# Performance work log

Hardware: AMD Instinct MI355X
Metric: run time of the kernel (lower is better)

## Reference

```python
import jax, jax.numpy as jnp
import numpy as np

NEG_INF = float(np.finfo(np.float32).min)


def setup_inputs() -> dict:
    key = jax.random.key(0)
    k1, k2, k3 = jax.random.split(key, 3)
    n_context, d_model = 4096, 2048
    x = jax.random.normal(k1, (n_context, d_model), dtype=jnp.float32)
    # nn.Linear default init scale ~ 1/sqrt(fan_in); use small weights for numeric sanity
    W_qk = jax.random.normal(k2, (d_model, d_model), dtype=jnp.float32) / np.sqrt(d_model)
    W_ov = jax.random.normal(k3, (d_model, d_model), dtype=jnp.float32) / np.sqrt(d_model)
    return {"x": x, "W_qk": W_qk, "W_ov": W_ov}


def reference(x, W_qk, W_ov):
    # Faithful to: softmax(X @ W_qk.T @ X.T + causal_mask) @ X @ W_ov.T
    # (biases of the torch Linears are never used in forward)
    n = x.shape[0]
    q = x @ W_qk.T                      # [n, d]
    scores = q @ x.T                    # [n, n]  (no 1/sqrt(d) scaling, as in source)
    causal = jnp.tril(jnp.ones((n, n), dtype=bool))
    scores = jnp.where(causal, scores, NEG_INF)  # additive -inf mask equivalent
    attn = jax.nn.softmax(scores, axis=-1)       # [n, n]
    out = (attn @ x) @ W_ov.T                    # [n, d]
    return out
```

## Files before the change

kernel.cpp:

```cpp
#include <hip/hip_runtime.h>
#include <hip/hip_bf16.h>
#include <stdint.h>
#include <stddef.h>
#include <math.h>

typedef _Float16 f16;
typedef __attribute__((ext_vector_type(8))) _Float16 f16x8;
typedef __attribute__((ext_vector_type(4))) float    f32x4;

constexpr int BM = 128, BN = 128, BK = 64;

#define GLOAD_LDS16(gp, lp)                                        \
    __builtin_amdgcn_global_load_lds(                              \
        (const __attribute__((address_space(1))) unsigned int*)(gp),\
        (__attribute__((address_space(3))) unsigned int*)(lp), 16, 0, 0)

#define MFMA_TILE(AV, BV)                                                     \
    do {                                                                      \
        __builtin_amdgcn_s_setprio(1);                                        \
        _Pragma("unroll")                                                     \
        for (int mi_ = 0; mi_ < 4; ++mi_)                                     \
            _Pragma("unroll")                                                 \
            for (int ni_ = 0; ni_ < 4; ++ni_)                                 \
                acc[mi_][ni_] = __builtin_amdgcn_mfma_f32_16x16x32_f16(       \
                    (AV)[mi_], (BV)[ni_], acc[mi_][ni_], 0, 0, 0);            \
        __builtin_amdgcn_s_setprio(0);                                        \
    } while (0)

#define SGB __builtin_amdgcn_sched_group_barrier

template <int EPI>
__global__ __launch_bounds__(512, 2) void gemm8_a2(
    const f16* __restrict__ Ah, const f16* __restrict__ Al,
    const f16* __restrict__ B,
    float* __restrict__ Cf, f16* __restrict__ Co, f16* __restrict__ Clo,
    int M, int N, int K)
{
    const int gx  = gridDim.x;
    const int nwg = gx * gridDim.y;
    const int id  = blockIdx.y * gx + blockIdx.x;
    const int cpx = nwg >> 3;
    const int j   = (id & 7) * cpx + (id >> 3);
    const int bx  = j % gx;
    const int by  = j / gx;

    const int tid   = threadIdx.x;
    const int lane  = tid & 63;
    const int wave  = tid >> 6;
    const int wm    = wave >> 2;
    const int wn    = wave & 3;
    const int lrow  = lane & 15;
    const int lquad = lane >> 4;

    __shared__ f16 lds[2][32768];

    const int row0 = by * 128;
    const int col0 = bx * 256;

    const int srow = tid >> 3;
    const int scol = ((tid & 7) ^ (srow & 7)) * 8;
    const int loff = wave * 512;

    const int g0 = ((lquad)     ^ (lrow & 7)) * 8;
    const int g1 = ((4 + lquad) ^ (lrow & 7)) * 8;

    const int arow = (wm * 64 + lrow) * 64;
    const int brow = (wn * 64 + lrow) * 64 + 16384;

    const f16* gAh = Ah + (size_t)(row0 + srow) * K + scol;
    const f16* gAl = Al + (size_t)(row0 + srow) * K + scol;
    const f16* gB  = B  + (size_t)(col0 + srow) * K + scol;
    const size_t r64 = (size_t)64 * K;

    f32x4 acc[4][4];
    const f32x4 fz = {0.f, 0.f, 0.f, 0.f};
    #pragma unroll
    for (int i = 0; i < 4; ++i)
        #pragma unroll
        for (int jj = 0; jj < 4; ++jj) acc[i][jj] = fz;

    const int nt = K / 64;

    #pragma unroll
    for (int u = 0; u < 4; ++u)
        GLOAD_LDS16(gB + u * r64, &lds[0][16384 + u * 4096 + loff]);
    #pragma unroll
    for (int u = 0; u < 2; ++u)
        GLOAD_LDS16(gAh + u * r64, &lds[0][u * 4096 + loff]);
    #pragma unroll
    for (int u = 0; u < 2; ++u)
        GLOAD_LDS16(gAl + u * r64, &lds[0][8192 + u * 4096 + loff]);
    asm volatile("s_waitcnt vmcnt(0)");
    __builtin_amdgcn_s_barrier();

    for (int t = 0; t < nt; ++t) {
        const f16* bufc = &lds[t & 1][0];
        f16* bufn = &lds[(t + 1) & 1][0];
        const size_t kn = (size_t)((t + 1 < nt) ? t + 1 : t) * 64;

        f16x8 ah0[4], ah1[4], al0[4], al1[4], bv0[4], bv1[4];

        #pragma unroll
        for (int mi = 0; mi < 4; ++mi)
            ah0[mi] = *(const f16x8*)&bufc[arow + mi * 1024 + g0];
        #pragma unroll
        for (int ni = 0; ni < 4; ++ni)
            bv0[ni] = *(const f16x8*)&bufc[brow + ni * 1024 + g0];

        GLOAD_LDS16(gB + kn,           &bufn[16384 + loff]);
        GLOAD_LDS16(gB + r64 + kn,     &bufn[16384 +  4096 + loff]);
        GLOAD_LDS16(gB + 2 * r64 + kn, &bufn[16384 +  8192 + loff]);
        GLOAD_LDS16(gB + 3 * r64 + kn, &bufn[16384 + 12288 + loff]);
        GLOAD_LDS16(gAh + kn,          &bufn[loff]);
        GLOAD_LDS16(gAh + r64 + kn,    &bufn[4096 + loff]);
        GLOAD_LDS16(gAl + kn,          &bufn[ 8192 + loff]);
        GLOAD_LDS16(gAl + r64 + kn,    &bufn[12288 + loff]);

        #pragma unroll
        for (int mi = 0; mi < 4; ++mi)
            ah1[mi] = *(const f16x8*)&bufc[arow + mi * 1024 + g1];
        #pragma unroll
        for (int ni = 0; ni < 4; ++ni)
            bv1[ni] = *(const f16x8*)&bufc[brow + ni * 1024 + g1];

        MFMA_TILE(ah0, bv0);

        #pragma unroll
        for (int mi = 0; mi < 4; ++mi)
            al0[mi] = *(const f16x8*)&bufc[8192 + arow + mi * 1024 + g0];

        MFMA_TILE(ah1, bv1);

        #pragma unroll
        for (int mi = 0; mi < 4; ++mi)
            al1[mi] = *(const f16x8*)&bufc[8192 + arow + mi * 1024 + g1];

        MFMA_TILE(al0, bv0);
        MFMA_TILE(al1, bv1);

        SGB(0x100, 8, 0);
        SGB(0x20,  8, 0);
        SGB(0x100, 8, 0);
        SGB(0x8,  16, 0);
        SGB(0x100, 4, 0);
        SGB(0x8,  16, 0);
        SGB(0x100, 4, 0);
        SGB(0x8,  32, 0);

        asm volatile("s_waitcnt vmcnt(0)");
        __builtin_amdgcn_s_barrier();
    }

    #pragma unroll
    for (int mi = 0; mi < 4; ++mi) {
        #pragma unroll
        for (int ni = 0; ni < 4; ++ni) {
            #pragma unroll
            for (int r = 0; r < 4; ++r) {
                const int row = row0 + wm * 64 + mi * 16 + lquad * 4 + r;
                const int col = col0 + wn * 64 + ni * 16 + lrow;
                const size_t idx = (size_t)row * N + col;
                const float v = acc[mi][ni][r];
                if (EPI == 0) {
                    Cf[idx] = v;
                } else {
                    const f16 h = (f16)v;
                    Co[idx]  = h;
                    Clo[idx] = (f16)(v - (float)h);
                }
            }
        }
    }
}

__global__ __launch_bounds__(512, 2) void gemm8_s_jobs(
    const f16* __restrict__ Ah, const f16* __restrict__ Al,
    const f16* __restrict__ B,
    float* __restrict__ Cf, int N, int K)
{
    const int b = blockIdx.x;
    const int j = (b & 7) * 32 + (b >> 3);
    int r = (int)sqrtf((float)j);
    while (r * r > j) --r;
    while ((r + 1) * (r + 1) <= j) ++r;
    const int u = j - r * r;
    const int by = (u < r) ? 2 * r : 2 * r + 1;
    const int bx = (u < r) ? u : u - r;

    const int tid   = threadIdx.x;
    const int lane  = tid & 63;
    const int wave  = tid >> 6;
    const int wm    = wave >> 2;
    const int wn    = wave & 3;
    const int lrow  = lane & 15;
    const int lquad = lane >> 4;

    __shared__ f16 lds[2][32768];

    const int row0 = by * 128;
    const int col0 = bx * 256;

    const int srow = tid >> 3;
    const int scol = ((tid & 7) ^ (srow & 7)) * 8;
    const int loff = wave * 512;

    const int g0 = ((lquad)     ^ (lrow & 7)) * 8;
    const int g1 = ((4 + lquad) ^ (lrow & 7)) * 8;

    const int arow = (wm * 64 + lrow) * 64;
    const int brow = (wn * 64 + lrow) * 64 + 16384;

    const f16* gAh = Ah + (size_t)(row0 + srow) * K + scol;
    const f16* gAl = Al + (size_t)(row0 + srow) * K + scol;
    const f16* gB  = B  + (size_t)(col0 + srow) * K + scol;
    const size_t r64 = (size_t)64 * K;

    f32x4 acc[4][4];
    const f32x4 fz = {0.f, 0.f, 0.f, 0.f};
    #pragma unroll
    for (int i = 0; i < 4; ++i)
        #pragma unroll
        for (int jj = 0; jj < 4; ++jj) acc[i][jj] = fz;

    const int nt = K / 64;

    #pragma unroll
    for (int u2 = 0; u2 < 4; ++u2)
        GLOAD_LDS16(gB + u2 * r64, &lds[0][16384 + u2 * 4096 + loff]);
    #pragma unroll
    for (int u2 = 0; u2 < 2; ++u2)
        GLOAD_LDS16(gAh + u2 * r64, &lds[0][u2 * 4096 + loff]);
    #pragma unroll
    for (int u2 = 0; u2 < 2; ++u2)
        GLOAD_LDS16(gAl + u2 * r64, &lds[0][8192 + u2 * 4096 + loff]);
    asm volatile("s_waitcnt vmcnt(0)");
    __builtin_amdgcn_s_barrier();

    for (int t = 0; t < nt; ++t) {
        const f16* bufc = &lds[t & 1][0];
        f16* bufn = &lds[(t + 1) & 1][0];
        const size_t kn = (size_t)((t + 1 < nt) ? t + 1 : t) * 64;

        f16x8 ah0[4], ah1[4], al0[4], al1[4], bv0[4], bv1[4];

        #pragma unroll
        for (int mi = 0; mi < 4; ++mi)
            ah0[mi] = *(const f16x8*)&bufc[arow + mi * 1024 + g0];
        #pragma unroll
        for (int ni = 0; ni < 4; ++ni)
            bv0[ni] = *(const f16x8*)&bufc[brow + ni * 1024 + g0];

        GLOAD_LDS16(gB + kn,           &bufn[16384 + loff]);
        GLOAD_LDS16(gB + r64 + kn,     &bufn[16384 +  4096 + loff]);
        GLOAD_LDS16(gB + 2 * r64 + kn, &bufn[16384 +  8192 + loff]);
        GLOAD_LDS16(gB + 3 * r64 + kn, &bufn[16384 + 12288 + loff]);
        GLOAD_LDS16(gAh + kn,          &bufn[loff]);
        GLOAD_LDS16(gAh + r64 + kn,    &bufn[4096 + loff]);
        GLOAD_LDS16(gAl + kn,          &bufn[ 8192 + loff]);
        GLOAD_LDS16(gAl + r64 + kn,    &bufn[12288 + loff]);

        #pragma unroll
        for (int mi = 0; mi < 4; ++mi)
            ah1[mi] = *(const f16x8*)&bufc[arow + mi * 1024 + g1];
        #pragma unroll
        for (int ni = 0; ni < 4; ++ni)
            bv1[ni] = *(const f16x8*)&bufc[brow + ni * 1024 + g1];

        MFMA_TILE(ah0, bv0);

        #pragma unroll
        for (int mi = 0; mi < 4; ++mi)
            al0[mi] = *(const f16x8*)&bufc[8192 + arow + mi * 1024 + g0];

        MFMA_TILE(ah1, bv1);

        #pragma unroll
        for (int mi = 0; mi < 4; ++mi)
            al1[mi] = *(const f16x8*)&bufc[8192 + arow + mi * 1024 + g1];

        MFMA_TILE(al0, bv0);
        MFMA_TILE(al1, bv1);

        SGB(0x100, 8, 0);
        SGB(0x20,  8, 0);
        SGB(0x100, 8, 0);
        SGB(0x8,  16, 0);
        SGB(0x100, 4, 0);
        SGB(0x8,  16, 0);
        SGB(0x100, 4, 0);
        SGB(0x8,  32, 0);

        asm volatile("s_waitcnt vmcnt(0)");
        __builtin_amdgcn_s_barrier();
    }

    #pragma unroll
    for (int mi = 0; mi < 4; ++mi) {
        #pragma unroll
        for (int ni = 0; ni < 4; ++ni) {
            #pragma unroll
            for (int rr = 0; rr < 4; ++rr) {
                const int row = row0 + wm * 64 + mi * 16 + lquad * 4 + rr;
                const int col = col0 + wn * 64 + ni * 16 + lrow;
                Cf[(size_t)row * N + col] = acc[mi][ni][rr];
            }
        }
    }
}

__global__ __launch_bounds__(256) void gemm_half_splitk(
    const f16* __restrict__ Ah, const f16* __restrict__ Al,
    const f16* __restrict__ B, float* __restrict__ Spart, int Kg)
{
    const int kc = blockIdx.x;
    const int h  = blockIdx.y;
    const int row0 = h * 256;
    const int kbeg = kc * 256;

    const int tid   = threadIdx.x;
    const int lane  = tid & 63;
    const int wave  = tid >> 6;
    const int wm    = wave >> 1;
    const int wn    = wave & 1;
    const int lrow  = lane & 15;
    const int lquad = lane >> 4;

    __shared__ f16 sAh[BM * BK];
    __shared__ f16 sAl[BM * BK];
    __shared__ f16 sB [BM * BK];

    const int srow = tid >> 3;
    const int scol = (((tid & 7) ^ ((tid >> 3) & 7))) * 8;
    const int lbase = wave * 512;

    f32x4 acc[4][4];
    const f32x4 fz = {0.f, 0.f, 0.f, 0.f};
    #pragma unroll
    for (int i = 0; i < 4; ++i)
        #pragma unroll
        for (int jj = 0; jj < 4; ++jj) acc[i][jj] = fz;

    for (int k0 = kbeg; k0 < kbeg + 256; k0 += BK) {
        __syncthreads();
        #pragma unroll
        for (int r = 0; r < 4; ++r) {
            const int trow = srow + 32 * r;
            const size_t ga = (size_t)(row0 + trow) * Kg + k0 + scol;
            const int ldst = lbase + r * 2048;
            GLOAD_LDS16(&Ah[ga], &sAh[ldst]);
            GLOAD_LDS16(&Al[ga], &sAl[ldst]);
            GLOAD_LDS16(&B [ga], &sB [ldst]);
        }
        __syncthreads();

        #pragma unroll
        for (int kk = 0; kk < 2; ++kk) {
            const int grpA = ((kk * 4 + lquad) ^ (lrow & 7)) * 8;
            f16x8 ah[4], al[4], bv[4];
            #pragma unroll
            for (int mi = 0; mi < 4; ++mi) {
                const int off = (wm * 64 + mi * 16 + lrow) * BK + grpA;
                ah[mi] = *reinterpret_cast<const f16x8*>(&sAh[off]);
                al[mi] = *reinterpret_cast<const f16x8*>(&sAl[off]);
            }
            #pragma unroll
            for (int ni = 0; ni < 4; ++ni)
                bv[ni] = *reinterpret_cast<const f16x8*>(
                    &sB[(wn * 64 + ni * 16 + lrow) * BK + grpA]);

            #pragma unroll
            for (int mi = 0; mi < 4; ++mi)
                #pragma unroll
                for (int ni = 0; ni < 4; ++ni) {
                    acc[mi][ni] = __builtin_amdgcn_mfma_f32_16x16x32_f16(
                        ah[mi], bv[ni], acc[mi][ni], 0, 0, 0);
                    acc[mi][ni] = __builtin_amdgcn_mfma_f32_16x16x32_f16(
                        al[mi], bv[ni], acc[mi][ni], 0, 0, 0);
                }
        }
    }

    float* outp = Spart + ((size_t)(kc * 16 + h)) * (128 * 128);
    #pragma unroll
    for (int mi = 0; mi < 4; ++mi) {
        #pragma unroll
        for (int ni = 0; ni < 4; ++ni) {
            #pragma unroll
            for (int r = 0; r < 4; ++r) {
                const int row = wm * 64 + mi * 16 + lquad * 4 + r;
                const int col = wn * 64 + ni * 16 + lrow;
                outp[row * 128 + col] = acc[mi][ni][r];
            }
        }
    }
}

__global__ __launch_bounds__(256) void combine_halves(
    const float* __restrict__ Spart, float* __restrict__ S, int n)
{
    const int h = blockIdx.y;
    const int e = (blockIdx.x * 256 + threadIdx.x) * 4;
    float4 a = *reinterpret_cast<const float4*>(
        &Spart[(size_t)h * (128 * 128) + e]);
    #pragma unroll
    for (int kc = 1; kc < 8; ++kc) {
        const float4 b = *reinterpret_cast<const float4*>(
            &Spart[(size_t)(kc * 16 + h) * (128 * 128) + e]);
        a.x += b.x; a.y += b.y; a.z += b.z; a.w += b.w;
    }
    const int i = e >> 7, jj = e & 127;
    *reinterpret_cast<float4*>(&S[(size_t)(h * 256 + i) * n + h * 256 + jj]) = a;
}

template <int EPI, bool KCAUSAL>
__global__ __launch_bounds__(512, 2) void gemm8_1t(
    const f16* __restrict__ A, const f16* __restrict__ B,
    float* __restrict__ Cf, f16* __restrict__ Co,
    int M, int N, int K)
{
    int bx, by;
    if (KCAUSAL) {
        bx = blockIdx.x;
        by = (int)gridDim.y - 1 - (int)blockIdx.y;
    } else {
        const int gx  = gridDim.x;
        const int nwg = gx * gridDim.y;
        const int id  = blockIdx.y * gx + blockIdx.x;
        const int cpx = nwg >> 3;
        const int j   = (id & 7) * cpx + (id >> 3);
        bx = j % gx;
        by = j / gx;
    }

    const int tid   = threadIdx.x;
    const int lane  = tid & 63;
    const int wave  = tid >> 6;
    const int wm    = wave >> 2;
    const int wn    = wave & 3;
    const int lrow  = lane & 15;
    const int lquad = lane >> 4;

    __shared__ f16 lds[3][24576];

    const int row0 = by * 128;
    const int col0 = bx * 256;

    const int srow = tid >> 3;
    const int scol = ((tid & 7) ^ (srow & 7)) * 8;
    const int loff = wave * 512;
    const int g0 = ((lquad)     ^ (lrow & 7)) * 8;
    const int g1 = ((4 + lquad) ^ (lrow & 7)) * 8;
    const int arow = (wm * 64 + lrow) * 64;
    const int brow = (wn * 64 + lrow) * 64 + 8192;

    const f16* gA = A + (size_t)(row0 + srow) * K + scol;
    const f16* gB = B + (size_t)(col0 + srow) * K + scol;
    const size_t r64 = (size_t)64 * K;

    f32x4 acc[4][4];
    const f32x4 fz = {0.f, 0.f, 0.f, 0.f};
    #pragma unroll
    for (int i = 0; i < 4; ++i)
        #pragma unroll
        for (int j2 = 0; j2 < 4; ++j2) acc[i][j2] = fz;

    const int Keff = KCAUSAL ? (by + 1) * 128 : K;
    const int nt = Keff / 64;

    #pragma unroll
    for (int tt = 0; tt < 2; ++tt) {
        const size_t kk = (size_t)tt * 64;
        #pragma unroll
        for (int u = 0; u < 4; ++u)
            GLOAD_LDS16(gB + u * r64 + kk, &lds[tt][8192 + u * 4096 + loff]);
        #pragma unroll
        for (int u = 0; u < 2; ++u)
            GLOAD_LDS16(gA + u * r64 + kk, &lds[tt][u * 4096 + loff]);
    }
    asm volatile("s_waitcnt vmcnt(6)");
    __builtin_amdgcn_s_barrier();

    int cur = 0;
    for (int t = 0; t < nt; ++t) {
        const int nb = (cur >= 1) ? (cur - 1) : (cur + 2);
        const size_t kn = (size_t)((t + 2 < nt) ? t + 2 : nt - 1) * 64;
        const f16* bufc = &lds[cur][0];
        f16* bufn = &lds[nb][0];

        f16x8 av0[4], av1[4], bv0[4], bv1[4];

        #pragma unroll
        for (int mi = 0; mi < 4; ++mi)
            av0[mi] = *(const f16x8*)&bufc[arow + mi * 1024 + g0];
        #pragma unroll
        for (int ni = 0; ni < 4; ++ni)
            bv0[ni] = *(const f16x8*)&bufc[brow + ni * 1024 + g0];

        GLOAD_LDS16(gB + kn,           &bufn[8192 + loff]);
        GLOAD_LDS16(gB + r64 + kn,     &bufn[8192 +  4096 + loff]);
        GLOAD_LDS16(gB + 2 * r64 + kn, &bufn[8192 +  8192 + loff]);
        GLOAD_LDS16(gB + 3 * r64 + kn, &bufn[8192 + 12288 + loff]);
        GLOAD_LDS16(gA + kn,           &bufn[loff]);
        GLOAD_LDS16(gA + r64 + kn,     &bufn[4096 + loff]);

        #pragma unroll
        for (int mi = 0; mi < 4; ++mi)
            av1[mi] = *(const f16x8*)&bufc[arow + mi * 1024 + g1];
        #pragma unroll
        for (int ni = 0; ni < 4; ++ni)
            bv1[ni] = *(const f16x8*)&bufc[brow + ni * 1024 + g1];

        MFMA_TILE(av0, bv0);
        MFMA_TILE(av1, bv1);

        SGB(0x100, 8, 0);
        SGB(0x20,  6, 0);
        SGB(0x100, 8, 0);
        SGB(0x8,  32, 0);

        asm volatile("s_waitcnt vmcnt(6)");
        __builtin_amdgcn_s_barrier();

        cur = (cur == 2) ? 0 : cur + 1;
    }

    #pragma unroll
    for (int mi = 0; mi < 4; ++mi) {
        #pragma unroll
        for (int ni = 0; ni < 4; ++ni) {
            #pragma unroll
            for (int r = 0; r < 4; ++r) {
                const int row = row0 + wm * 64 + mi * 16 + lquad * 4 + r;
                const int col = col0 + wn * 64 + ni * 16 + lrow;
                const size_t idx = (size_t)row * N + col;
                const float v = acc[mi][ni][r];
                if (EPI == 0) Cf[idx] = v;
                else          Co[idx] = (f16)v;
            }
        }
    }
}

__global__ __launch_bounds__(256) void split_f32_f16(
    const float* __restrict__ in, f16* __restrict__ hi, f16* __restrict__ lo,
    size_t nelem)
{
    const size_t i = ((size_t)blockIdx.x * 256 + threadIdx.x) * 4;
    if (i >= nelem) return;
    const float4 v = *reinterpret_cast<const float4*>(in + i);
    union { f16 h[4]; ushort4 u; } H, L;
    H.h[0] = (f16)v.x; H.h[1] = (f16)v.y; H.h[2] = (f16)v.z; H.h[3] = (f16)v.w;
    *reinterpret_cast<ushort4*>(hi + i) = H.u;
    if (lo) {
        L.h[0] = (f16)(v.x - (float)H.h[0]);
        L.h[1] = (f16)(v.y - (float)H.h[1]);
        L.h[2] = (f16)(v.z - (float)H.h[2]);
        L.h[3] = (f16)(v.w - (float)H.h[3]);
        *reinterpret_cast<ushort4*>(lo + i) = L.u;
    }
}

__global__ __launch_bounds__(256) void prep_x(
    const float* __restrict__ in, f16* __restrict__ hi, f16* __restrict__ lo,
    f16* __restrict__ tr, int rows, int cols)
{
    __shared__ float tile[32][33];
    const int bx = blockIdx.x;
    const int by = blockIdx.y;
    const int tx = threadIdx.x & 31;
    const int ty = threadIdx.x >> 5;
    #pragma unroll
    for (int r = 0; r < 4; ++r) {
        const int row = by * 32 + ty + 8 * r;
        const int col = bx * 32 + tx;
        const float v = in[(size_t)row * cols + col];
        tile[ty + 8 * r][tx] = v;
        const f16 h = (f16)v;
        hi[(size_t)row * cols + col] = h;
        lo[(size_t)row * cols + col] = (f16)(v - (float)h);
    }
    __syncthreads();
    #pragma unroll
    for (int r = 0; r < 4; ++r)
        tr[(size_t)(bx * 32 + ty + 8 * r) * rows + by * 32 + tx] =
            (f16)tile[tx][ty + 8 * r];
}

__global__ __launch_bounds__(256) void softmax_rows(
    const float* __restrict__ S, f16* __restrict__ P, int n)
{
    const int row = blockIdx.x;
    const int len = row + 1;
    const int padlen = ((row >> 7) + 1) << 7;
    const float* srow = S + (size_t)row * n;
    f16* prow = P + (size_t)row * n;
    const int tid = threadIdx.x;
    const int lane = tid & 63, wave = tid >> 6;
    __shared__ float rowbuf[4096];
    __shared__ float redm[4], reds[4];

    float m = -3.0e38f, s = 0.f;
    for (int j = tid; j < len; j += 256) {
        const float v = srow[j];
        rowbuf[j] = v;
        const float mn = fmaxf(m, v);
        s = s * __expf(m - mn) + __expf(v - mn);
        m = mn;
    }
    #pragma unroll
    for (int off = 32; off; off >>= 1) {
        const float mo = __shfl_xor(m, off, 64);
        const float so = __shfl_xor(s, off, 64);
        const float mn = fmaxf(m, mo);
        s = s * __expf(m - mn) + so * __expf(mo - mn);
        m = mn;
    }
    if (lane == 0) { redm[wave] = m; reds[wave] = s; }
    __syncthreads();
    float M = redm[0], Sm = reds[0];
    #pragma unroll
    for (int w = 1; w < 4; ++w) {
        const float mn = fmaxf(M, redm[w]);
        Sm = Sm * __expf(M - mn) + reds[w] * __expf(redm[w] - mn);
        M = mn;
    }
    const float inv = 1.0f / Sm;

    const f16 z = (f16)0.0f;
    for (int j = tid; j < padlen; j += 256)
        prow[j] = (j < len) ? (f16)(__expf(rowbuf[j] - M) * inv) : z;
}

extern "C" void kernel_launch(void* const* d_in, const int* in_sizes, int n_in,
                              void* d_out, int out_size, void* d_ws, size_t ws_size,
                              hipStream_t stream)
{
    const int n = 4096, d = 2048;
    const float* x   = (const float*)d_in[0];
    const float* Wqk = (const float*)d_in[1];
    const float* Wov = (const float*)d_in[2];
    float* out = (float*)d_out;

    char* ws = (char*)d_ws;
    const size_t MB = 1 << 20;
    f16*   xh   = (f16*)  (ws);
    f16*   xl   = (f16*)  (ws + 16 * MB);
    f16*   Wh   = (f16*)  (ws + 32 * MB);
    f16*   Wovh = (f16*)  (ws + 40 * MB);
    f16*   xTh  = (f16*)  (ws + 48 * MB);
    f16*   qh   = (f16*)  (ws + 64 * MB);
    f16*   ql   = (f16*)  (ws + 80 * MB);
    float* S    = (float*)(ws + 96 * MB);
    float* Sp   = (float*)(ws + 16 * MB);
    f16*   P    = (f16*)  (ws);
    f16*   o    = (f16*)  (ws + 64 * MB);

    const dim3 blk(256);
    const dim3 blk8(512);

    split_f32_f16<<<dim3((d * d) / (256 * 4)), blk, 0, stream>>>(Wqk, Wh, nullptr, (size_t)d * d);
    split_f32_f16<<<dim3((d * d) / (256 * 4)), blk, 0, stream>>>(Wov, Wovh, nullptr, (size_t)d * d);
    prep_x<<<dim3(d / 32, n / 32), blk, 0, stream>>>(x, xh, xl, xTh, n, d);

    gemm8_a2<1><<<dim3(d / 256, n / 128), blk8, 0, stream>>>(
        xh, xl, Wh, nullptr, qh, ql, n, d, d);

    gemm8_s_jobs<<<dim3(256), blk8, 0, stream>>>(qh, ql, xh, S, n, d);
    gemm_half_splitk<<<dim3(8, 16), blk, 0, stream>>>(qh, ql, xh, Sp, d);
    combine_halves<<<dim3(16, 16), blk, 0, stream>>>(Sp, S, n);

    softmax_rows<<<dim3(n), blk, 0, stream>>>(S, P, n);

    gemm8_1t<2, true><<<dim3(d / 256, n / 128), blk8, 0, stream>>>(
        P, xTh, nullptr, o, n, d, n);

    gemm8_1t<0, false><<<dim3(d / 256, n / 128), blk8, 0, stream>>>(
        o, Wovh, out, nullptr, n, d, d);
}
```

Measured before the change: 367.2 us.

## Load B operand directly from global into registers, bypassing LDS staging

Both GEMM kernels stop staging the B tile through shared memory. Each wave now reads its B fragments straight from global memory into registers at the current k-step, which halves the LDS footprint and may allow higher occupancy. Only the Ah/Al tiles remain double-buffered in LDS, and the sched_group_barrier pattern is reworked to match. The risk is that the B global loads are issued in the same iteration they are consumed, with no prefetch, so their latency can stall the MFMAs. B data also gets no reuse across the waves that share the same column block.

```diff
diff --git a/kernel.cpp b/kernel.cpp
--- a/kernel.cpp
+++ b/kernel.cpp
@@ -52,7 +52,7 @@
     const int lrow  = lane & 15;
     const int lquad = lane >> 4;
 
-    __shared__ f16 lds[2][32768];
+    __shared__ f16 lds[2][16384];
 
     const int row0 = by * 128;
     const int col0 = bx * 256;
@@ -65,12 +65,12 @@
     const int g1 = ((4 + lquad) ^ (lrow & 7)) * 8;
 
     const int arow = (wm * 64 + lrow) * 64;
-    const int brow = (wn * 64 + lrow) * 64 + 16384;
 
     const f16* gAh = Ah + (size_t)(row0 + srow) * K + scol;
     const f16* gAl = Al + (size_t)(row0 + srow) * K + scol;
-    const f16* gB  = B  + (size_t)(col0 + srow) * K + scol;
+    const f16* gBr = B + (size_t)(col0 + wn * 64 + lrow) * K + lquad * 8;
     const size_t r64 = (size_t)64 * K;
+    const size_t r16 = (size_t)16 * K;
 
     f32x4 acc[4][4];
     const f32x4 fz = {0.f, 0.f, 0.f, 0.f};
@@ -81,15 +81,10 @@
 
     const int nt = K / 64;
 
-    #pragma unroll
-    for (int u = 0; u < 4; ++u)
-        GLOAD_LDS16(gB + u * r64, &lds[0][16384 + u * 4096 + loff]);
-    #pragma unroll
-    for (int u = 0; u < 2; ++u)
-        GLOAD_LDS16(gAh + u * r64, &lds[0][u * 4096 + loff]);
-    #pragma unroll
-    for (int u = 0; u < 2; ++u)
-        GLOAD_LDS16(gAl + u * r64, &lds[0][8192 + u * 4096 + loff]);
+    GLOAD_LDS16(gAh,       &lds[0][loff]);
+    GLOAD_LDS16(gAh + r64, &lds[0][4096 + loff]);
+    GLOAD_LDS16(gAl,       &lds[0][8192 + loff]);
+    GLOAD_LDS16(gAl + r64, &lds[0][12288 + loff]);
     asm volatile("s_waitcnt vmcnt(0)");
     __builtin_amdgcn_s_barrier();
 
@@ -97,55 +92,46 @@
         const f16* bufc = &lds[t & 1][0];
         f16* bufn = &lds[(t + 1) & 1][0];
         const size_t kn = (size_t)((t + 1 < nt) ? t + 1 : t) * 64;
+        const size_t kb = (size_t)t * 64;
 
         f16x8 ah0[4], ah1[4], al0[4], al1[4], bv0[4], bv1[4];
 
         #pragma unroll
+        for (int ni = 0; ni < 4; ++ni)
+            bv0[ni] = *(const f16x8*)(gBr + (size_t)ni * r16 + kb);
+        #pragma unroll
+        for (int ni = 0; ni < 4; ++ni)
+            bv1[ni] = *(const f16x8*)(gBr + (size_t)ni * r16 + kb + 32);
+
+        #pragma unroll
         for (int mi = 0; mi < 4; ++mi)
             ah0[mi] = *(const f16x8*)&bufc[arow + mi * 1024 + g0];
-        #pragma unroll
-        for (int ni = 0; ni < 4; ++ni)
-            bv0[ni] = *(const f16x8*)&bufc[brow + ni * 1024 + g0];
-
-        GLOAD_LDS16(gB + kn,           &bufn[16384 + loff]);
-        GLOAD_LDS16(gB + r64 + kn,     &bufn[16384 +  4096 + loff]);
-        GLOAD_LDS16(gB + 2 * r64 + kn, &bufn[16384 +  8192 + loff]);
-        GLOAD_LDS16(gB + 3 * r64 + kn, &bufn[16384 + 12288 + loff]);
-        GLOAD_LDS16(gAh + kn,          &bufn[loff]);
-        GLOAD_LDS16(gAh + r64 + kn,    &bufn[4096 + loff]);
-        GLOAD_LDS16(gAl + kn,          &bufn[ 8192 + loff]);
-        GLOAD_LDS16(gAl + r64 + kn,    &bufn[12288 + loff]);
+
+        GLOAD_LDS16(gAh + kn,       &bufn[loff]);
+        GLOAD_LDS16(gAh + r64 + kn, &bufn[4096 + loff]);
+        GLOAD_LDS16(gAl + kn,       &bufn[ 8192 + loff]);
+        GLOAD_LDS16(gAl + r64 + kn, &bufn[12288 + loff]);
 
         #pragma unroll
         for (int mi = 0; mi < 4; ++mi)
             ah1[mi] = *(const f16x8*)&bufc[arow + mi * 1024 + g1];
         #pragma unroll
-        for (int ni = 0; ni < 4; ++ni)
-            bv1[ni] = *(const f16x8*)&bufc[brow + ni * 1024 + g1];
+        for (int mi = 0; mi < 4; ++mi)
+            al0[mi] = *(const f16x8*)&bufc[8192 + arow + mi * 1024 + g0];
+        #pragma unroll
+        for (int mi = 0; mi < 4; ++mi)
+            al1[mi] = *(const f16x8*)&bufc[8192 + arow + mi * 1024 + g1];
 
         MFMA_TILE(ah0, bv0);
-
-        #pragma unroll
-        for (int mi = 0; mi < 4; ++mi)
-            al0[mi] = *(const f16x8*)&bufc[8192 + arow + mi * 1024 + g0];
-
         MFMA_TILE(ah1, bv1);
-
-        #pragma unroll
-        for (int mi = 0; mi < 4; ++mi)
-            al1[mi] = *(const f16x8*)&bufc[8192 + arow + mi * 1024 + g1];
-
         MFMA_TILE(al0, bv0);
         MFMA_TILE(al1, bv1);
 
-        SGB(0x100, 8, 0);
         SGB(0x20,  8, 0);
-        SGB(0x100, 8, 0);
-        SGB(0x8,  16, 0);
         SGB(0x100, 4, 0);
-        SGB(0x8,  16, 0);
-        SGB(0x100, 4, 0);
-        SGB(0x8,  32, 0);
+        SGB(0x20,  4, 0);
+        SGB(0x100, 12, 0);
+        SGB(0x8,  64, 0);
 
         asm volatile("s_waitcnt vmcnt(0)");
         __builtin_amdgcn_s_barrier();
@@ -195,7 +181,7 @@
     const int lrow  = lane & 15;
     const int lquad = lane >> 4;
 
-    __shared__ f16 lds[2][32768];
+    __shared__ f16 lds[2][16384];
 
     const int row0 = by * 128;
     const int col0 = bx * 256;
@@ -208,12 +194,12 @@
     const int g1 = ((4 + lquad) ^ (lrow & 7)) * 8;
 
     const int arow = (wm * 64 + lrow) * 64;
-    const int brow = (wn * 64 + lrow) * 64 + 16384;
 
     const f16* gAh = Ah + (size_t)(row0 + srow) * K + scol;
     const f16* gAl = Al + (size_t)(row0 + srow) * K + scol;
-    const f16* gB  = B  + (size_t)(col0 + srow) * K + scol;
+    const f16* gBr = B + (size_t)(col0 + wn * 64 + lrow) * K + lquad * 8;
     const size_t r64 = (size_t)64 * K;
+    const size_t r16 = (size_t)16 * K;
 
     f32x4 acc[4][4];
     const f32x4 fz = {0.f, 0.f, 0.f, 0.f};
@@ -224,15 +210,10 @@
 
     const int nt = K / 64;
 
-    #pragma unroll
-    for (int u2 = 0; u2 < 4; ++u2)
-        GLOAD_LDS16(gB + u2 * r64, &lds[0][16384 + u2 * 4096 + loff]);
-    #pragma unroll
-    for (int u2 = 0; u2 < 2; ++u2)
-        GLOAD_LDS16(gAh + u2 * r64, &lds[0][u2 * 4096 + loff]);
-    #pragma unroll
-    for (int u2 = 0; u2 < 2; ++u2)
-        GLOAD_LDS16(gAl + u2 * r64, &lds[0][8192 + u2 * 4096 + loff]);
+    GLOAD_LDS16(gAh,       &lds[0][loff]);
+    GLOAD_LDS16(gAh + r64, &lds[0][4096 + loff]);
+    GLOAD_LDS16(gAl,       &lds[0][8192 + loff]);
+    GLOAD_LDS16(gAl + r64, &lds[0][12288 + loff]);
     asm volatile("s_waitcnt vmcnt(0)");
     __builtin_amdgcn_s_barrier();
 
@@ -240,55 +221,46 @@
         const f16* bufc = &lds[t & 1][0];
         f16* bufn = &lds[(t + 1) & 1][0];
         const size_t kn = (size_t)((t + 1 < nt) ? t + 1 : t) * 64;
+        const size_t kb = (size_t)t * 64;
 
         f16x8 ah0[4], ah1[4], al0[4], al1[4], bv0[4], bv1[4];
 
         #pragma unroll
+        for (int ni = 0; ni < 4; ++ni)
+            bv0[ni] = *(const f16x8*)(gBr + (size_t)ni * r16 + kb);
+        #pragma unroll
+        for (int ni = 0; ni < 4; ++ni)
+            bv1[ni] = *(const f16x8*)(gBr + (size_t)ni * r16 + kb + 32);
+
+        #pragma unroll
         for (int mi = 0; mi < 4; ++mi)
             ah0[mi] = *(const f16x8*)&bufc[arow + mi * 1024 + g0];
-        #pragma unroll
-        for (int ni = 0; ni < 4; ++ni)
-            bv0[ni] = *(const f16x8*)&bufc[brow + ni * 1024 + g0];
-
-        GLOAD_LDS16(gB + kn,           &bufn[16384 + loff]);
-        GLOAD_LDS16(gB + r64 + kn,     &bufn[16384 +  4096 + loff]);
-        GLOAD_LDS16(gB + 2 * r64 + kn, &bufn[16384 +  8192 + loff]);
-        GLOAD_LDS16(gB + 3 * r64 + kn, &bufn[16384 + 12288 + loff]);
-        GLOAD_LDS16(gAh + kn,          &bufn[loff]);
-        GLOAD_LDS16(gAh + r64 + kn,    &bufn[4096 + loff]);
-        GLOAD_LDS16(gAl + kn,          &bufn[ 8192 + loff]);
-        GLOAD_LDS16(gAl + r64 + kn,    &bufn[12288 + loff]);
+
+        GLOAD_LDS16(gAh + kn,       &bufn[loff]);
+        GLOAD_LDS16(gAh + r64 + kn, &bufn[4096 + loff]);
+        GLOAD_LDS16(gAl + kn,       &bufn[ 8192 + loff]);
+        GLOAD_LDS16(gAl + r64 + kn, &bufn[12288 + loff]);
 
         #pragma unroll
         for (int mi = 0; mi < 4; ++mi)
             ah1[mi] = *(const f16x8*)&bufc[arow + mi * 1024 + g1];
         #pragma unroll
-        for (int ni = 0; ni < 4; ++ni)
-            bv1[ni] = *(const f16x8*)&bufc[brow + ni * 1024 + g1];
+        for (int mi = 0; mi < 4; ++mi)
+            al0[mi] = *(const f16x8*)&bufc[8192 + arow + mi * 1024 + g0];
+        #pragma unroll
+        for (int mi = 0; mi < 4; ++mi)
+            al1[mi] = *(const f16x8*)&bufc[8192 + arow + mi * 1024 + g1];
 
         MFMA_TILE(ah0, bv0);
-
-        #pragma unroll
-        for (int mi = 0; mi < 4; ++mi)
-            al0[mi] = *(const f16x8*)&bufc[8192 + arow + mi * 1024 + g0];
-
         MFMA_TILE(ah1, bv1);
-
-        #pragma unroll
-        for (int mi = 0; mi < 4; ++mi)
-            al1[mi] = *(const f16x8*)&bufc[8192 + arow + mi * 1024 + g1];
-
         MFMA_TILE(al0, bv0);
         MFMA_TILE(al1, bv1);
 
-        SGB(0x100, 8, 0);
         SGB(0x20,  8, 0);
-        SGB(0x100, 8, 0);
-        SGB(0x8,  16, 0);
         SGB(0x100, 4, 0);
-        SGB(0x8,  16, 0);
-        SGB(0x100, 4, 0);
-        SGB(0x8,  32, 0);
+        SGB(0x20,  4, 0);
+        SGB(0x100, 12, 0);
+        SGB(0x8,  64, 0);
 
         asm volatile("s_waitcnt vmcnt(0)");
         __builtin_amdgcn_s_barrier();
```

Measured after the change: 435.4 us. 18.6% more time.
